# Kernel optimization log

Measured on AMD Instinct MI355X. Metric: run time of the kernel, lower is better.

Reference implementation:

```python
import jax, jax.numpy as jnp
import numpy as np

THRESHOLD = 1.0
DECAY = 0.95
T, B, N_IN = 16, 512, 3072
S1, S2, S3 = 256, 256, 128
E = 8


def _lif_step(v, h):
    # LIF membrane update: decay, integrate, threshold-spike, soft reset.
    v = v * DECAY + h
    spk = (v >= THRESHOLD).astype(v.dtype)
    return spk, v - spk * THRESHOLD


def setup_inputs() -> dict:
    key = jax.random.key(0)
    k_seq, k1, k2, k3 = jax.random.split(key, 4)
    # Binary spike train input (rate-coded), shape (T, B, N_in)
    spike_seq = (jax.random.uniform(k_seq, (T, B, N_IN)) < 0.5).astype(jnp.float32)
    # Expert weights: nn.Linear weight layout is (out, in); init N(0, 0.05)
    W1 = 0.05 * jax.random.normal(k1, (E, S1, N_IN), dtype=jnp.float32)
    W2 = 0.05 * jax.random.normal(k2, (E, S2, S1), dtype=jnp.float32)
    W3 = 0.05 * jax.random.normal(k3, (E, S3, S2), dtype=jnp.float32)
    # Uniform gates 1/num_experts (requires_grad=False buffers in the original)
    g = jnp.full((E,), 1.0 / E, dtype=jnp.float32)
    return {"spike_seq": spike_seq, "W1": W1, "W2": W2, "W3": W3,
            "g1": g, "g2": g, "g3": g}


def reference(spike_seq, W1, W2, W3, g1, g2, g3):
    t, b = spike_seq.shape[0], spike_seq.shape[1]
    x = spike_seq.reshape(t, b, -1)
    e = W1.shape[0]
    dt = x.dtype
    v1 = jnp.zeros((e, b, W1.shape[1]), dt)
    v2 = jnp.zeros((e, b, W2.shape[1]), dt)
    v3 = jnp.zeros((e, b, W3.shape[1]), dt)

    def step(carry, xt):
        v1, v2, v3 = carry
        # stage 1: batched per-expert GEMM + LIF + gated combine
        h1 = jnp.einsum('bi,eoi->ebo', xt, W1)
        spk1, v1 = _lif_step(v1, h1)
        c1 = jnp.einsum('e,ebo->bo', g1, spk1)
        # stage 2
        h2 = jnp.einsum('bi,eoi->ebo', c1, W2)
        spk2, v2 = _lif_step(v2, h2)
        c2 = jnp.einsum('e,ebo->bo', g2, spk2)
        # stage 3
        h3 = jnp.einsum('bi,eoi->ebo', c2, W3)
        spk3, v3 = _lif_step(v3, h3)
        c3 = jnp.einsum('e,ebo->bo', g3, spk3)
        return (v1, v2, v3), (c1, c2, c3)

    _, (s1, s2, s3) = jax.lax.scan(step, (v1, v2, v3), x)
    # time-averaged combined outputs per stage
    return s1.mean(axis=0), s2.mean(axis=0), s3.mean(axis=0)
```

## Files before the change

### kernel.cpp

```cpp
#include <hip/hip_runtime.h>
#include <hip/hip_bf16.h>
#include <cmath>

#define T_STEPS 16
#define BATCH   512
#define N_IN    3072
#define S1      256
#define S2      256
#define S3      128
#define NEXP    8
#define M_ROWS  (T_STEPS * BATCH)
#define MT_ALL  (M_ROWS / 32)

typedef int v4i  __attribute__((ext_vector_type(4)));
typedef int v16i __attribute__((ext_vector_type(16)));
typedef unsigned long long u64;
typedef unsigned int uint32;

__device__ __forceinline__ v4i unpack16_bits(uint32 w16)
{
    v4i d;
    #pragma unroll
    for (int c = 0; c < 4; ++c) {
        uint32 x = (w16 >> (4 * c)) & 0xFu;
        x = x + (x << 7);
        x = x + (x << 14);
        d[c] = (int)(x & 0x01010101u);
    }
    return d;
}

template<int S, int K>
__device__ __forceinline__ void digitize_chunk(
    const float* __restrict__ W, char* __restrict__ Bf, int t)
{
    int lane16 = t & 63;
    int o  = (t >> 6) & (S - 1);
    int kb = t >> ((S == 256) ? 14 : 13);
    int r  = lane16 & 31;
    int qd = lane16 >> 5;
    int e    = r >> 2;
    int limb = r & 3;
    int k0 = kb * 32 + qd * 16;

    const float4* Wp = (const float4*)(W + ((size_t)e * S + o) * K + k0);
    char out[16];
    #pragma unroll
    for (int f4 = 0; f4 < 4; ++f4) {
        float4 w = Wp[f4];
        float ws[4] = {w.x, w.y, w.z, w.w};
        #pragma unroll
        for (int c = 0; c < 4; ++c) {
            long long q = llrint((double)ws[c] * 4294967296.0);
            int d = 0;
            #pragma unroll
            for (int l = 0; l < 4; ++l) {
                int dl = (int)((q + 128) & 255) - 128;
                q = (q - dl) >> 8;
                if (l == limb) d = dl;
            }
            out[f4 * 4 + c] = (char)d;
        }
    }
    *(v4i*)(Bf + (size_t)t * 16) = *(v4i*)out;
}

__global__ __launch_bounds__(256) void prep(
    const float* __restrict__ x,  const float* __restrict__ W1,
    const float* __restrict__ W2, const float* __restrict__ W3,
    u64* __restrict__ bitsT, char* __restrict__ B1f,
    char* __restrict__ B2f,  char* __restrict__ B3f)
{
    const int bid = blockIdx.x;
    const int tid = threadIdx.x;
    if (bid < 98304) {
        int gid = bid * 256 + tid;
        float v = x[gid];
        u64 m = __ballot(v >= 0.5f);
        if ((tid & 63) == 0) {
            int tb = gid / N_IN;
            int k  = gid - tb * N_IN;
            int t  = tb >> 9;
            int b  = tb & 511;
            bitsT[(size_t)(k >> 6) * M_ROWS + (b * 16 + t)] = m;
        }
    } else if (bid < 98304 + 4608) {
        int t    = (bid - 98304) * 256 + tid;
        int l16  = t & 63;
        int tt   = t >> 6;
        int tile = tt % 192;
        int kb   = tt / 192;
        int gr   = tile * 32 + (l16 & 31);
        int qd   = l16 >> 5;
        int limb = gr >> 11;
        int oe   = gr & 2047;
        int o    = oe >> 3;
        int e    = oe & 7;
        int k0   = kb * 32 + qd * 16;
        const float4* Wp = (const float4*)(W1 + ((size_t)e * S1 + o) * N_IN + k0);
        char out[16];
        #pragma unroll
        for (int f4 = 0; f4 < 4; ++f4) {
            float4 w = Wp[f4];
            float ws[4] = {w.x, w.y, w.z, w.w};
            #pragma unroll
            for (int c = 0; c < 4; ++c) {
                long long q = llrint((double)ws[c] * 16777216.0);
                int d0 = (int)((q + 128) & 255) - 128;
                long long q1 = (q - d0) >> 8;
                int d1 = (int)((q1 + 128) & 255) - 128;
                int d2 = (int)((q1 - d1) >> 8);
                int d  = (limb == 0) ? d0 : ((limb == 1) ? d1 : d2);
                out[f4 * 4 + c] = (char)d;
            }
        }
        *(v4i*)(B1f + (size_t)t * 16) = *(v4i*)out;
    } else if (bid < 98304 + 4608 + 512) {
        digitize_chunk<S2, S1>(W2, B2f, (bid - 98304 - 4608) * 256 + tid);
    } else {
        digitize_chunk<S3, S2>(W3, B3f, (bid - 98304 - 4608 - 512) * 256 + tid);
    }
}

__global__ __launch_bounds__(256, 4) void fused_stage1(
    const u64* __restrict__ AT0, const char* __restrict__ Bf,
    const float* __restrict__ g, char* __restrict__ Cf,
    float* __restrict__ Mean)
{
    constexpr int KI      = N_IN / 64;
    constexpr int KSTRIDE = 192 * 1024;
    constexpr int BSTEP   = 2 * KSTRIDE;
    __shared__ double hs[128 * 32];

    const int tid  = threadIdx.x;
    const int lane = tid & 63;
    const int w    = tid >> 6;
    const int col  = lane & 31;
    const int qd   = lane >> 5;
    const int wm   = w * 32;

    const int id    = blockIdx.x;
    const int xcd   = id & 7;
    const int inner = id >> 3;
    const int nblk  = xcd * 8 + (inner >> 6);
    const int mblk  = inner & 63;
    const int m0    = mblk * 128;

    const u64* AT = AT0 + (m0 + wm + col);
    const int sh16 = qd * 16;
    const char* Bu = Bf + (size_t)nblk * 1024 + lane * 16;

    v16i acc[3];
    #pragma unroll
    for (int j = 0; j < 3; ++j)
        #pragma unroll
        for (int r = 0; r < 16; ++r) acc[j][r] = 0;

    u64 ab[2];
    v4i Bb[2][6];

    ab[0] = AT[0];
    #pragma unroll
    for (int ks = 0; ks < 2; ++ks)
        #pragma unroll
        for (int jj = 0; jj < 3; ++jj)
            Bb[0][ks * 3 + jj] =
                *(const v4i*)(Bu + ks * KSTRIDE + jj * 65536);

    auto body = [&](int it, int cur, int pf) {
        const int itp = it + 1;
        ab[pf] = AT[(size_t)itp * M_ROWS];
        const char* bu = Bu + (size_t)itp * BSTEP;
        #pragma unroll
        for (int ks = 0; ks < 2; ++ks)
            #pragma unroll
            for (int jj = 0; jj < 3; ++jj)
                Bb[pf][ks * 3 + jj] =
                    *(const v4i*)(bu + ks * KSTRIDE + jj * 65536);
        __builtin_amdgcn_s_setprio(1);
        #pragma unroll
        for (int ks = 0; ks < 2; ++ks) {
            uint32 dw = ks ? (uint32)(ab[cur] >> 32) : (uint32)ab[cur];
            v4i af = unpack16_bits(dw >> sh16);
            #pragma unroll
            for (int jj = 0; jj < 3; ++jj)
                acc[jj] = __builtin_amdgcn_mfma_i32_32x32x32_i8(
                    af, Bb[cur][ks * 3 + jj], acc[jj], 0, 0, 0);
        }
        __builtin_amdgcn_s_setprio(0);
    };

    for (int it = 0; it < KI; it += 2) {
        body(it + 0, 0, 1);
        body(it + 1, 1, 0);
    }

    const double sc = 1.0 / 16777216.0;
    #pragma unroll
    for (int reg = 0; reg < 16; ++reg) {
        int m  = wm + (reg & 3) + 8 * (reg >> 2) + 4 * qd;
        int lo = acc[0][reg] + (acc[1][reg] << 8);
        double d = ((double)lo + 65536.0 * (double)acc[2][reg]) * sc;
        hs[m * 32 + col] = d;
    }
    __syncthreads();

    const int b_loc = tid >> 5;
    const int oe    = tid & 31;
    const int o_loc = oe >> 3;
    const int e     = tid & 7;
    const float ge  = g[e];
    const int bg = mblk * 8 + b_loc;
    const int og = nblk * 4 + o_loc;

    const int kb_a   = og >> 5;
    const int qd_a   = (og >> 4) & 1;
    const int byte_a = og & 15;

    double v = 0.0;
    float gacc = 0.0f;
    #pragma unroll
    for (int t = 0; t < T_STEPS; ++t) {
        double h  = hs[(b_loc * 16 + t) * 32 + oe];
        double vv = v * 0.95 + h;
        int spk = (vv >= 1.0) ? 1 : 0;
        v = vv - (double)spk;
        float gs = ge * (float)spk;
        gs += __shfl_xor(gs, 1);
        gs += __shfl_xor(gs, 2);
        gs += __shfl_xor(gs, 4);
        gacc += gs;
        int cnt = spk;
        cnt += __shfl_xor(cnt, 1);
        cnt += __shfl_xor(cnt, 2);
        cnt += __shfl_xor(cnt, 4);
        if (e == 0) {
            int mp = bg * 16 + t;
            int lane_a = (mp & 31) + 32 * qd_a;
            Cf[(((size_t)kb_a * MT_ALL + (mp >> 5)) * 64 + lane_a) * 16 + byte_a]
                = (char)cnt;
        }
    }
    if (e == 0) Mean[(size_t)bg * S1 + og] = gacc * 0.0625f;
}

template<int K, int S, int SHIFT, bool WRITEC, int NBLK, int MINW>
__global__ __launch_bounds__(256, MINW) void fused_stage(
    const char* __restrict__ Ap, const char* __restrict__ Bf,
    const float* __restrict__ g, char* __restrict__ Cf,
    float* __restrict__ Mean)
{
    constexpr int KI = K / 64;
    static_assert(KI % 2 == 0, "frag path wants even KI");
    constexpr int NT = S;
    constexpr int NS = NBLK / 8;
    __shared__ double hs[256][16];

    const int tid  = threadIdx.x;
    const int lane = tid & 63;
    const int w    = tid >> 6;
    const int col  = lane & 31;
    const int qd   = lane >> 5;
    const int wm   = w * 64;

    const int id    = blockIdx.x;
    const int xcd   = id & 7;
    const int inner = id >> 3;
    const int nblk  = xcd * NS + (inner >> 5);
    const int mblk  = inner & 31;
    const int m0    = mblk * 256;

    const int nt0 = nblk * 2;
    const char* Bbase = Bf + ((size_t)nt0 * 64 + lane) * 16;

    v16i acc[2][2];
    #pragma unroll
    for (int i = 0; i < 2; ++i)
        #pragma unroll
        for (int j = 0; j < 2; ++j)
            #pragma unroll
            for (int r = 0; r < 16; ++r) acc[i][j][r] = 0;

    auto loadB = [&](int kb, int jj) -> v4i {
        return *(const v4i*)(Bbase + (size_t)kb * (NT * 1024) + jj * 1024);
    };
    const int mt0 = (m0 + wm) >> 5;
    const char* Abase = Ap + ((size_t)mt0 * 64 + lane) * 16;
    auto loadA = [&](int kb, int ii) -> v4i {
        return *(const v4i*)(Abase + (size_t)kb * (MT_ALL * 1024) + ii * 1024);
    };

    v4i Ab[2][4];
    v4i Bb[2][4];

    #pragma unroll
    for (int ks = 0; ks < 2; ++ks) {
        Ab[0][ks * 2 + 0] = loadA(ks, 0);
        Ab[0][ks * 2 + 1] = loadA(ks, 1);
        #pragma unroll
        for (int jj = 0; jj < 2; ++jj)
            Bb[0][ks * 2 + jj] = loadB(ks, jj);
    }

    auto body = [&](int it, int cur, int pf) {
        const int itp = it + 1;
        #pragma unroll
        for (int ks = 0; ks < 2; ++ks) {
            Ab[pf][ks * 2 + 0] = loadA(itp * 2 + ks, 0);
            Ab[pf][ks * 2 + 1] = loadA(itp * 2 + ks, 1);
            #pragma unroll
            for (int jj = 0; jj < 2; ++jj)
                Bb[pf][ks * 2 + jj] = loadB(itp * 2 + ks, jj);
        }
        #pragma unroll
        for (int ks = 0; ks < 2; ++ks)
            #pragma unroll
            for (int jj = 0; jj < 2; ++jj) {
                acc[0][jj] = __builtin_amdgcn_mfma_i32_32x32x32_i8(Ab[cur][ks*2+0], Bb[cur][ks*2+jj], acc[0][jj], 0,0,0);
                acc[1][jj] = __builtin_amdgcn_mfma_i32_32x32x32_i8(Ab[cur][ks*2+1], Bb[cur][ks*2+jj], acc[1][jj], 0,0,0);
            }
    };
    for (int it = 0; it < KI; it += 2) {
        body(it + 0, 0, 1);
        body(it + 1, 1, 0);
    }

    const double sbase = 1.0 / (double)(1ll << SHIFT);
    #pragma unroll
    for (int j = 0; j < 2; ++j) {
        const int oe = j * 8 + (col >> 2);
        #pragma unroll
        for (int i = 0; i < 2; ++i) {
            #pragma unroll
            for (int reg = 0; reg < 16; ++reg) {
                int a = acc[i][j][reg];
                int s01 = a + (__shfl_xor(a, 1) << 8);
                int s23 = __shfl_xor(s01, 2);
                double d = ((double)s01 + 65536.0 * (double)s23) * sbase;
                if ((col & 3) == 0) {
                    int m = wm + i * 32 + (reg & 3) + 8 * (reg >> 2) + 4 * qd;
                    hs[m][oe] = d;
                }
            }
        }
    }
    __syncthreads();

    const int b_loc  = tid >> 4;
    const int o_loc  = (tid >> 3) & 1;
    const int e      = tid & 7;
    const int oe     = o_loc * 8 + e;
    const float ge   = g[e];
    const int bg = mblk * 16 + b_loc;
    const int og = nblk * 2 + o_loc;

    const int kb_a   = og >> 5;
    const int qd_a   = (og >> 4) & 1;
    const int byte_a = og & 15;

    double v = 0.0;
    float gacc = 0.0f;
    #pragma unroll
    for (int t = 0; t < T_STEPS; ++t) {
        double h  = hs[b_loc * 16 + t][oe];
        double vv = v * 0.95 + h;
        int spk = (vv >= 1.0) ? 1 : 0;
        v = vv - (double)spk;
        float gs = ge * (float)spk;
        gs += __shfl_xor(gs, 1);
        gs += __shfl_xor(gs, 2);
        gs += __shfl_xor(gs, 4);
        gacc += gs;
        if (WRITEC) {
            int cnt = spk;
            cnt += __shfl_xor(cnt, 1);
            cnt += __shfl_xor(cnt, 2);
            cnt += __shfl_xor(cnt, 4);
            if (e == 0) {
                int mp = bg * 16 + t;
                int lane_a = (mp & 31) + 32 * qd_a;
                Cf[(((size_t)kb_a * MT_ALL + (mp >> 5)) * 64 + lane_a) * 16 + byte_a]
                    = (char)cnt;
            }
        }
    }
    if (e == 0) Mean[(size_t)bg * S + og] = gacc * 0.0625f;
}

extern "C" void kernel_launch(void* const* d_in, const int* in_sizes, int n_in,
                              void* d_out, int out_size, void* d_ws, size_t ws_size,
                              hipStream_t stream) {
    const float* x  = (const float*)d_in[0];
    const float* W1 = (const float*)d_in[1];
    const float* W2 = (const float*)d_in[2];
    const float* W3 = (const float*)d_in[3];
    const float* g1 = (const float*)d_in[4];
    const float* g2 = (const float*)d_in[5];
    const float* g3 = (const float*)d_in[6];
    float* out = (float*)d_out;

    char* ws = (char*)d_ws;
    u64*  AbitsT = (u64*)ws;
    char* B1f    = ws + 4194304ull;
    char* B2f    = ws + 25165824ull;
    char* B3f    = ws + 28311552ull;
    char* c1f    = ws + 30408704ull;
    char* c2f    = ws + 34603008ull;

    dim3 blk(256);

    prep<<<98304 + 4608 + 512 + 256, blk, 0, stream>>>(
        x, W1, W2, W3, AbitsT, B1f, B2f, B3f);

    fused_stage1<<<64 * 64, blk, 0, stream>>>(AbitsT, B1f, g1, c1f, out);

    fused_stage<S1, S2, 35, true,  128, 3><<<32 * 128, blk, 0, stream>>>(
        c1f, B2f, g2, c2f, out + BATCH * S1);
    fused_stage<S2, S3, 35, false, 64, 3><<<32 * 64, blk, 0, stream>>>(
        c2f, B3f, g3, nullptr, out + BATCH * (S1 + S2));
}
```

Measured before the change: 500.2 us.

## Stage B fragments through LDS and double M tile per block in stage1

Stage1 now gives each block 256 rows instead of 128, with each wave computing two 32-row M tiles. The B weight fragments are staged cooperatively into double-buffered LDS using global_load_lds, so each block fetches them once and all four waves reuse them, instead of every wave loading B from global memory itself. The grid is halved and the LIF epilogue runs in two passes that reuse the same shared buffer. The cost is more accumulator registers (launch bounds drop from 4 to 3 waves per SIMD) plus block barriers on every K group.

```diff
diff --git a/kernel.cpp b/kernel.cpp
--- a/kernel.cpp
+++ b/kernel.cpp
@@ -122,126 +122,163 @@
     }
 }
 
-__global__ __launch_bounds__(256, 4) void fused_stage1(
+__global__ __launch_bounds__(256, 3) void fused_stage1(
     const u64* __restrict__ AT0, const char* __restrict__ Bf,
     const float* __restrict__ g, char* __restrict__ Cf,
     float* __restrict__ Mean)
 {
-    constexpr int KI      = N_IN / 64;
-    constexpr int KSTRIDE = 192 * 1024;
-    constexpr int BSTEP   = 2 * KSTRIDE;
-    __shared__ double hs[128 * 32];
+    constexpr int NGR = (N_IN / 32) / 4;
+    __shared__ char smem[32768];
+    double* hs  = (double*)smem;
+    char*  Blds = smem;
 
     const int tid  = threadIdx.x;
     const int lane = tid & 63;
     const int w    = tid >> 6;
     const int col  = lane & 31;
     const int qd   = lane >> 5;
-    const int wm   = w * 32;
+    const int sh16 = qd * 16;
 
     const int id    = blockIdx.x;
     const int xcd   = id & 7;
     const int inner = id >> 3;
-    const int nblk  = xcd * 8 + (inner >> 6);
-    const int mblk  = inner & 63;
-    const int m0    = mblk * 128;
-
-    const u64* AT = AT0 + (m0 + wm + col);
-    const int sh16 = qd * 16;
-    const char* Bu = Bf + (size_t)nblk * 1024 + lane * 16;
-
-    v16i acc[3];
-    #pragma unroll
-    for (int j = 0; j < 3; ++j)
-        #pragma unroll
-        for (int r = 0; r < 16; ++r) acc[j][r] = 0;
-
-    u64 ab[2];
-    v4i Bb[2][6];
-
-    ab[0] = AT[0];
-    #pragma unroll
-    for (int ks = 0; ks < 2; ++ks)
+    const int nblk  = xcd * 8 + (inner >> 5);
+    const int mblk  = inner & 31;
+    const int m0    = mblk * 256;
+
+    const u64* AT = AT0 + (m0 + w * 64 + col);
+
+    const char* Bsrc = Bf + (size_t)nblk * 1024 + lane * 16;
+    char* Bdst0 = Blds + (w * 3) * 1024 + lane * 16;
+
+    v16i acc[2][3];
+    #pragma unroll
+    for (int mt = 0; mt < 2; ++mt)
         #pragma unroll
         for (int jj = 0; jj < 3; ++jj)
-            Bb[0][ks * 3 + jj] =
-                *(const v4i*)(Bu + ks * KSTRIDE + jj * 65536);
-
-    auto body = [&](int it, int cur, int pf) {
-        const int itp = it + 1;
-        ab[pf] = AT[(size_t)itp * M_ROWS];
-        const char* bu = Bu + (size_t)itp * BSTEP;
-        #pragma unroll
-        for (int ks = 0; ks < 2; ++ks)
+            #pragma unroll
+            for (int r = 0; r < 16; ++r) acc[mt][jj][r] = 0;
+
+    u64 areg[2][4];
+
+    auto stageB = [&](int gr, int buf) {
+        const char* src = Bsrc + (size_t)(gr * 4 + w) * (192 * 1024);
+        char* dst = Bdst0 + buf * 12288;
+        #pragma unroll
+        for (int jj = 0; jj < 3; ++jj)
+            __builtin_amdgcn_global_load_lds(
+                (const __attribute__((address_space(1))) uint32*)(src + jj * 65536),
+                (__attribute__((address_space(3))) uint32*)(dst + jj * 1024),
+                16, 0, 0);
+    };
+    auto loadA = [&](int gr, int buf) {
+        const int kw = gr * 2;
+        areg[buf][0] = AT[(size_t)kw * M_ROWS];
+        areg[buf][1] = AT[(size_t)kw * M_ROWS + 32];
+        areg[buf][2] = AT[(size_t)(kw + 1) * M_ROWS];
+        areg[buf][3] = AT[(size_t)(kw + 1) * M_ROWS + 32];
+    };
+
+    stageB(0, 0);
+    loadA(0, 0);
+
+    auto iter = [&](int gr, int cur, int pf) {
+        stageB(gr + 1, pf);
+        loadA(gr + 1, pf);
+        asm volatile("s_waitcnt vmcnt(7)" ::: "memory");
+        __builtin_amdgcn_sched_barrier(0);
+        __builtin_amdgcn_s_barrier();
+        const char* bb = Blds + cur * 12288 + lane * 16;
+        __builtin_amdgcn_s_setprio(1);
+        #pragma unroll
+        for (int kbl = 0; kbl < 4; ++kbl) {
+            v4i Bfr[3];
             #pragma unroll
             for (int jj = 0; jj < 3; ++jj)
-                Bb[pf][ks * 3 + jj] =
-                    *(const v4i*)(bu + ks * KSTRIDE + jj * 65536);
-        __builtin_amdgcn_s_setprio(1);
-        #pragma unroll
-        for (int ks = 0; ks < 2; ++ks) {
-            uint32 dw = ks ? (uint32)(ab[cur] >> 32) : (uint32)ab[cur];
-            v4i af = unpack16_bits(dw >> sh16);
-            #pragma unroll
-            for (int jj = 0; jj < 3; ++jj)
-                acc[jj] = __builtin_amdgcn_mfma_i32_32x32x32_i8(
-                    af, Bb[cur][ks * 3 + jj], acc[jj], 0, 0, 0);
+                Bfr[jj] = *(const v4i*)(bb + (kbl * 3 + jj) * 1024);
+            const int kwl = kbl >> 1;
+            v4i af[2];
+            #pragma unroll
+            for (int mt = 0; mt < 2; ++mt) {
+                u64 a = areg[cur][kwl * 2 + mt];
+                uint32 dw = (kbl & 1) ? (uint32)(a >> 32) : (uint32)a;
+                af[mt] = unpack16_bits(dw >> sh16);
+            }
+            #pragma unroll
+            for (int mt = 0; mt < 2; ++mt)
+                #pragma unroll
+                for (int jj = 0; jj < 3; ++jj)
+                    acc[mt][jj] = __builtin_amdgcn_mfma_i32_32x32x32_i8(
+                        af[mt], Bfr[jj], acc[mt][jj], 0, 0, 0);
         }
         __builtin_amdgcn_s_setprio(0);
-    };
-
-    for (int it = 0; it < KI; it += 2) {
-        body(it + 0, 0, 1);
-        body(it + 1, 1, 0);
+        __builtin_amdgcn_s_barrier();
+    };
+
+    for (int gp = 0; gp < NGR; gp += 2) {
+        iter(gp + 0, 0, 1);
+        iter(gp + 1, 1, 0);
     }
 
     const double sc = 1.0 / 16777216.0;
-    #pragma unroll
-    for (int reg = 0; reg < 16; ++reg) {
-        int m  = wm + (reg & 3) + 8 * (reg >> 2) + 4 * qd;
-        int lo = acc[0][reg] + (acc[1][reg] << 8);
-        double d = ((double)lo + 65536.0 * (double)acc[2][reg]) * sc;
-        hs[m * 32 + col] = d;
-    }
-    __syncthreads();
-
+    auto write_hs = [&](int wl) {
+        #pragma unroll
+        for (int mt = 0; mt < 2; ++mt)
+            #pragma unroll
+            for (int reg = 0; reg < 16; ++reg) {
+                int r  = wl * 64 + mt * 32 + (reg & 3) + 8 * (reg >> 2) + 4 * qd;
+                int lo = acc[mt][0][reg] + (acc[mt][1][reg] << 8);
+                double d = ((double)lo + 65536.0 * (double)acc[mt][2][reg]) * sc;
+                hs[r * 32 + col] = d;
+            }
+    };
     const int b_loc = tid >> 5;
     const int oe    = tid & 31;
     const int o_loc = oe >> 3;
     const int e     = tid & 7;
     const float ge  = g[e];
-    const int bg = mblk * 8 + b_loc;
-    const int og = nblk * 4 + o_loc;
-
+    const int og    = nblk * 4 + o_loc;
     const int kb_a   = og >> 5;
     const int qd_a   = (og >> 4) & 1;
     const int byte_a = og & 15;
 
-    double v = 0.0;
-    float gacc = 0.0f;
-    #pragma unroll
-    for (int t = 0; t < T_STEPS; ++t) {
-        double h  = hs[(b_loc * 16 + t) * 32 + oe];
-        double vv = v * 0.95 + h;
-        int spk = (vv >= 1.0) ? 1 : 0;
-        v = vv - (double)spk;
-        float gs = ge * (float)spk;
-        gs += __shfl_xor(gs, 1);
-        gs += __shfl_xor(gs, 2);
-        gs += __shfl_xor(gs, 4);
-        gacc += gs;
-        int cnt = spk;
-        cnt += __shfl_xor(cnt, 1);
-        cnt += __shfl_xor(cnt, 2);
-        cnt += __shfl_xor(cnt, 4);
-        if (e == 0) {
-            int mp = bg * 16 + t;
-            int lane_a = (mp & 31) + 32 * qd_a;
-            Cf[(((size_t)kb_a * MT_ALL + (mp >> 5)) * 64 + lane_a) * 16 + byte_a]
-                = (char)cnt;
-        }
-    }
-    if (e == 0) Mean[(size_t)bg * S1 + og] = gacc * 0.0625f;
+    auto lif_pass = [&](int pass) {
+        const int bg = mblk * 16 + pass * 8 + b_loc;
+        double v = 0.0;
+        float gacc = 0.0f;
+        #pragma unroll
+        for (int t = 0; t < T_STEPS; ++t) {
+            double h  = hs[(b_loc * 16 + t) * 32 + oe];
+            double vv = v * 0.95 + h;
+            int spk = (vv >= 1.0) ? 1 : 0;
+            v = vv - (double)spk;
+            float gs = ge * (float)spk;
+            gs += __shfl_xor(gs, 1);
+            gs += __shfl_xor(gs, 2);
+            gs += __shfl_xor(gs, 4);
+            gacc += gs;
+            int cnt = spk;
+            cnt += __shfl_xor(cnt, 1);
+            cnt += __shfl_xor(cnt, 2);
+            cnt += __shfl_xor(cnt, 4);
+            if (e == 0) {
+                int mp = bg * 16 + t;
+                int lane_a = (mp & 31) + 32 * qd_a;
+                Cf[(((size_t)kb_a * MT_ALL + (mp >> 5)) * 64 + lane_a) * 16 + byte_a]
+                    = (char)cnt;
+            }
+        }
+        if (e == 0) Mean[(size_t)bg * S1 + og] = gacc * 0.0625f;
+    };
+
+    __syncthreads();
+    if (w < 2) write_hs(w);
+    __syncthreads();
+    lif_pass(0);
+    __syncthreads();
+    if (w >= 2) write_hs(w - 2);
+    __syncthreads();
+    lif_pass(1);
 }
 
 template<int K, int S, int SHIFT, bool WRITEC, int NBLK, int MINW>
@@ -412,7 +449,7 @@
     prep<<<98304 + 4608 + 512 + 256, blk, 0, stream>>>(
         x, W1, W2, W3, AbitsT, B1f, B2f, B3f);
 
-    fused_stage1<<<64 * 64, blk, 0, stream>>>(AbitsT, B1f, g1, c1f, out);
+    fused_stage1<<<32 * 64, blk, 0, stream>>>(AbitsT, B1f, g1, c1f, out);
 
     fused_stage<S1, S2, 35, true,  128, 3><<<32 * 128, blk, 0, stream>>>(
         c1f, B2f, g2, c2f, out + BATCH * S1);
```

After: 449.8 us. 10.1% less time.
